# Optimization experiments

Measured on AMD Instinct MI355X. Metric: run time of the kernel, lower is better.

Reference implementation:

```python
import jax, jax.numpy as jnp
import numpy as np

NEG_INF = -9e15
ALPHA = 0.2  # leaky relu slope


def setup_inputs() -> dict:
    key = jax.random.key(0)
    k1, k2, k3, k4 = jax.random.split(key, 4)
    B, N, Din = 8, 1024, 128
    H, D = 8, 16
    h = jax.random.normal(k1, (B, N, Din), dtype=jnp.float32)
    adj = jax.random.randint(k2, (B, N, N), 0, 2, dtype=jnp.int32)
    W = jax.random.normal(k3, (Din, H * D), dtype=jnp.float32) * 0.1
    a = jax.random.normal(k4, (H, 2 * D, 1), dtype=jnp.float32) * 0.1
    return {"h": h, "adj": adj, "W": W, "a": a}


def reference(h, adj, W, a):
    B, N, _ = h.shape
    H, twoD, _ = a.shape
    D = twoD // 2
    # Wh: [B, N, H, D]
    Wh = (h @ W).reshape(B, N, H, D)
    # Decompose additive attention: a . [Wh_i ; Wh_j] = a_src . Wh_i + a_dst . Wh_j
    a_src = a[:, :D, 0]   # [H, D]
    a_dst = a[:, D:, 0]   # [H, D]
    s_i = jnp.einsum('bnhd,hd->bhn', Wh, a_src)  # [B, H, N]
    s_j = jnp.einsum('bnhd,hd->bhn', Wh, a_dst)  # [B, H, N]
    scores = jax.nn.leaky_relu(s_i[:, :, :, None] + s_j[:, :, None, :], ALPHA)  # [B,H,N,N]
    scores = jnp.where(adj[:, None, :, :] == 0, NEG_INF, scores)
    attn = jax.nn.softmax(scores, axis=-1)  # [B, H, N, N]
    # Weighted aggregation over neighbors j
    h_prime = jnp.einsum('bhij,bjhd->bihd', attn, Wh).reshape(B, N, H * D)
    return h_prime
```

## Files before the change

kernel.cpp:

```cpp
#include <hip/hip_runtime.h>
#include <hip/hip_bf16.h>

constexpr int B   = 8;
constexpr int N   = 1024;
constexpr int DIN = 128;
constexpr int H   = 8;
constexpr int D   = 16;
constexpr int HD  = 128;
constexpr int TI  = 16;

#define LOG2E 1.4426950408889634f
#define TCLAMP 30.0f

typedef __attribute__((ext_vector_type(8))) short bf16x8;
typedef __attribute__((ext_vector_type(4))) float f32x4;

__device__ inline float fast_exp2(float x) {
#if __has_builtin(__builtin_amdgcn_exp2f)
    return __builtin_amdgcn_exp2f(x);
#else
    return exp2f(x);
#endif
}

__global__ __launch_bounds__(256) void k_proj(
    const float* __restrict__ hsrc,
    const float* __restrict__ W,
    const float* __restrict__ a,
    __hip_bfloat16* __restrict__ WhT,
    float* __restrict__ tI,
    float* __restrict__ tJ)
{
    const int row0 = blockIdx.x * 16;
    const int b    = row0 >> 10;
    const int n0   = row0 & (N - 1);
    const int t    = threadIdx.x;
    const int lane = t & 63, wave = t >> 6;
    const int mn   = lane & 15, kg = lane >> 4;

    __shared__ __align__(16) __hip_bfloat16 hA[16][136];
    __shared__ __align__(16) __hip_bfloat16 Wt[128][136];

    {
        const float4* hf = reinterpret_cast<const float4*>(hsrc + (size_t)row0 * DIN);
        #pragma unroll
        for (int u = 0; u < 2; ++u) {
            const int idx = t + u * 256;
            const float4 v = hf[idx];
            const int r = idx >> 5, c4 = (idx & 31) * 4;
            hA[r][c4]     = __float2bfloat16(v.x);
            hA[r][c4 + 1] = __float2bfloat16(v.y);
            hA[r][c4 + 2] = __float2bfloat16(v.z);
            hA[r][c4 + 3] = __float2bfloat16(v.w);
        }
    }
    {
        const float4* wf = reinterpret_cast<const float4*>(W);
        #pragma unroll
        for (int u = 0; u < 16; ++u) {
            const int idx = t + u * 256;
            const float4 v = wf[idx];
            const int k = idx >> 5, c0 = (idx & 31) * 4;
            Wt[c0][k]     = __float2bfloat16(v.x);
            Wt[c0 + 1][k] = __float2bfloat16(v.y);
            Wt[c0 + 2][k] = __float2bfloat16(v.z);
            Wt[c0 + 3][k] = __float2bfloat16(v.w);
        }
    }
    __syncthreads();

    f32x4 acc[2];
    acc[0] = (f32x4){0.f, 0.f, 0.f, 0.f};
    acc[1] = (f32x4){0.f, 0.f, 0.f, 0.f};

    #pragma unroll
    for (int kk = 0; kk < 4; ++kk) {
        const bf16x8 af = *reinterpret_cast<const bf16x8*>(
            &hA[mn][kk * 32 + kg * 8]);
        #pragma unroll
        for (int f = 0; f < 2; ++f) {
            const int F = wave * 2 + f;
            const bf16x8 bfr = *reinterpret_cast<const bf16x8*>(
                &Wt[F * 16 + mn][kk * 32 + kg * 8]);
            acc[f] = __builtin_amdgcn_mfma_f32_16x16x32_bf16(af, bfr, acc[f], 0, 0, 0);
        }
    }

    #pragma unroll
    for (int f = 0; f < 2; ++f) {
        const int F = wave * 2 + f;
        const float as = a[F * 32 + mn];
        const float ad = a[F * 32 + 16 + mn];
        #pragma unroll
        for (int r = 0; r < 4; ++r) {
            const int n = n0 + kg * 4 + r;
            WhT[((size_t)(b * HD + F * 16 + mn)) * N + n] =
                __float2bfloat16(acc[f][r]);
            float vi = acc[f][r] * as;
            float vj = acc[f][r] * ad;
            #pragma unroll
            for (int m = 1; m < 16; m <<= 1) {
                vi += __shfl_xor(vi, m);
                vj += __shfl_xor(vj, m);
            }
            if (mn == 0) {
                tI[((size_t)(b * H + F)) * N + n] = fminf(vi * LOG2E, TCLAMP);
                tJ[((size_t)(b * H + F)) * N + n] = fminf(vj * LOG2E, TCLAMP);
            }
        }
    }
}

__global__ __launch_bounds__(512, 4) void k_attn(
    const int*            __restrict__ adj,
    const __hip_bfloat16* __restrict__ WhT,
    const float*          __restrict__ tI,
    const float*          __restrict__ tJ,
    float*                __restrict__ out)
{
    const int b    = blockIdx.y;
    const int i0   = blockIdx.x * TI;
    const int t    = threadIdx.x;
    const int lane = t & 63, h = t >> 6;
    const int mn   = lane & 15, kg = lane >> 4;

    __shared__ unsigned int m2[32][16];

    {
        const int* ar = adj + ((size_t)(b * N) + i0 + 2 * h) * N + lane;
        #pragma unroll
        for (int rr = 0; rr < 2; ++rr) {
            #pragma unroll
            for (int tt = 0; tt < 16; ++tt) {
                const int v = ar[rr * N + tt * 64];
                const unsigned long long mm = __ballot(v != 0);
                if (lane == 0)
                    m2[2 * tt][2 * h + rr] = (unsigned int)mm;
                if (lane == 32)
                    m2[2 * tt + 1][2 * h + rr] = (unsigned int)(mm >> 32);
            }
        }
    }
    __syncthreads();

    const float Arow = tI[((size_t)(b * H + h)) * N + i0 + mn];
    const float* tjrow = tJ + ((size_t)(b * H + h)) * N + kg * 8;
    const __hip_bfloat16* wrow =
        WhT + ((size_t)(b * HD + h * 16 + mn)) * N + kg * 8;

    f32x4 accO = {0.f, 0.f, 0.f, 0.f};
    f32x4 accD = {0.f, 0.f, 0.f, 0.f};
    bf16x8 ones;
    #pragma unroll
    for (int e = 0; e < 8; ++e) ones[e] = (short)0x3F80;

    for (int sq = 0; sq < 8; ++sq) {
        const int j0 = sq * 128;

        unsigned int mvq[4];
        #pragma unroll
        for (int q = 0; q < 4; ++q) mvq[q] = m2[sq * 4 + q][mn];
        float4 ta[4], tb[4]; bf16x8 wv[4];
        #pragma unroll
        for (int q = 0; q < 4; ++q) {
            ta[q] = *reinterpret_cast<const float4*>(tjrow + j0 + q * 32);
            tb[q] = *reinterpret_cast<const float4*>(tjrow + j0 + q * 32 + 4);
            wv[q] = *reinterpret_cast<const bf16x8*>(wrow + j0 + q * 32);
        }

        #pragma unroll
        for (int q = 0; q < 4; ++q) {
            const unsigned int m8 = (mvq[q] >> (kg * 8)) & 0xFFu;
            const float tv[8] = {ta[q].x, ta[q].y, ta[q].z, ta[q].w,
                                 tb[q].x, tb[q].y, tb[q].z, tb[q].w};
            bf16x8 af;
            #pragma unroll
            for (int e = 0; e < 8; ++e) {
                const float x = Arow + tv[e];
                float sc = fmaxf(x, 0.2f * x);
                sc = ((m8 >> e) & 1u) ? sc : -1.0e30f;
                af[e] = (short)__bfloat16_as_ushort(
                    __float2bfloat16(fast_exp2(sc)));
            }
            accO = __builtin_amdgcn_mfma_f32_16x16x32_bf16(af, wv[q], accO, 0, 0, 0);
            accD = __builtin_amdgcn_mfma_f32_16x16x32_bf16(af, ones, accD, 0, 0, 0);
        }
    }

    #pragma unroll
    for (int r = 0; r < 4; ++r) {
        out[((size_t)(b * N) + i0 + kg * 4 + r) * HD + h * 16 + mn] =
            accO[r] / accD[r];
    }
}

extern "C" void kernel_launch(void* const* d_in, const int* in_sizes, int n_in,
                              void* d_out, int out_size, void* d_ws, size_t ws_size,
                              hipStream_t stream)
{
    const float* h   = (const float*)d_in[0];
    const int*   adj = (const int*)d_in[1];
    const float* W   = (const float*)d_in[2];
    const float* a   = (const float*)d_in[3];
    float* out = (float*)d_out;

    float* ws = (float*)d_ws;
    float* tI = ws;
    float* tJ = ws + (size_t)B * H * N;
    __hip_bfloat16* WhT = (__hip_bfloat16*)(ws + (size_t)2 * B * H * N);

    k_proj<<<dim3(B * N / 16), dim3(256), 0, stream>>>(h, W, a, WhT, tI, tJ);
    k_attn<<<dim3(N / TI, B), dim3(512), 0, stream>>>(adj, WhT, tI, tJ, out);
}
```

Baseline: 55.10 us.

## Pre-pack adjacency bitmask in separate kernel and double-buffer loads in attention

Adjacency ballot-packing moves out of the attention kernel into a dedicated k_pack kernel that writes a per-row 32-word bitmask. The attention kernel now reads this bitmask straight from global memory, with no shared memory or block barrier. Its grid is split over head halves to give 256-thread blocks. The j-loop is double-buffered with two register sets, and sched_barriers overlap the next chunk's loads with the current chunk's compute. This costs an extra kernel launch and more register pressure, and it drops the previous occupancy hint.

```diff
diff --git a/kernel.cpp b/kernel.cpp
--- a/kernel.cpp
+++ b/kernel.cpp
@@ -21,6 +21,21 @@
 #else
     return exp2f(x);
 #endif
+}
+
+__global__ __launch_bounds__(256) void k_pack(const int* __restrict__ adj,
+                                              unsigned int* __restrict__ bm)
+{
+    const int lane = threadIdx.x & 63;
+    const size_t row = (size_t)blockIdx.x * 4 + (threadIdx.x >> 6);
+    const int* ar = adj + row * N + lane;
+    unsigned int* dst = bm + row * 32;
+    #pragma unroll
+    for (int tt = 0; tt < 16; ++tt) {
+        const unsigned long long m = __ballot(ar[tt * 64] != 0);
+        if (lane == 0)  dst[2 * tt]     = (unsigned int)m;
+        if (lane == 32) dst[2 * tt + 1] = (unsigned int)(m >> 32);
+    }
 }
 
 __global__ __launch_bounds__(256) void k_proj(
@@ -111,8 +126,38 @@
     }
 }
 
-__global__ __launch_bounds__(512, 4) void k_attn(
-    const int*            __restrict__ adj,
+
+#define LOADSET(M, T0, T1, WV, SQ) do {                                        \
+    M = mrow[SQ];                                                              \
+    _Pragma("unroll")                                                          \
+    for (int q = 0; q < 4; ++q) {                                              \
+        T0[q] = *reinterpret_cast<const float4*>(tjrow + (SQ) * 128 + q * 32);     \
+        T1[q] = *reinterpret_cast<const float4*>(tjrow + (SQ) * 128 + q * 32 + 4); \
+        WV[q] = *reinterpret_cast<const bf16x8*>(wrow + (SQ) * 128 + q * 32);      \
+    } } while (0)
+
+#define COMPUTESET(M, T0, T1, WV) do {                                         \
+    const unsigned int mq_[4] = {M.x, M.y, M.z, M.w};                          \
+    _Pragma("unroll")                                                          \
+    for (int q = 0; q < 4; ++q) {                                              \
+        const unsigned int m8_ = (mq_[q] >> (kg * 8)) & 0xFFu;                 \
+        const float tv_[8] = {T0[q].x, T0[q].y, T0[q].z, T0[q].w,              \
+                              T1[q].x, T1[q].y, T1[q].z, T1[q].w};             \
+        bf16x8 af_;                                                            \
+        _Pragma("unroll")                                                      \
+        for (int e = 0; e < 8; ++e) {                                          \
+            const float x_ = Arow + tv_[e];                                    \
+            float sc_ = fmaxf(x_, 0.2f * x_);                                  \
+            sc_ = ((m8_ >> e) & 1u) ? sc_ : -1.0e30f;                          \
+            af_[e] = (short)__bfloat16_as_ushort(                              \
+                __float2bfloat16(fast_exp2(sc_)));                             \
+        }                                                                      \
+        accO = __builtin_amdgcn_mfma_f32_16x16x32_bf16(af_, WV[q], accO, 0, 0, 0); \
+        accD = __builtin_amdgcn_mfma_f32_16x16x32_bf16(af_, ones, accD, 0, 0, 0);  \
+    } } while (0)
+
+__global__ __launch_bounds__(256) void k_attn(
+    const unsigned int*   __restrict__ bm,
     const __hip_bfloat16* __restrict__ WhT,
     const float*          __restrict__ tI,
     const float*          __restrict__ tJ,
@@ -120,33 +165,17 @@
 {
     const int b    = blockIdx.y;
     const int i0   = blockIdx.x * TI;
-    const int t    = threadIdx.x;
-    const int lane = t & 63, h = t >> 6;
+    const int lane = threadIdx.x & 63;
+    const int h    = blockIdx.z * 4 + (threadIdx.x >> 6);
     const int mn   = lane & 15, kg = lane >> 4;
-
-    __shared__ unsigned int m2[32][16];
-
-    {
-        const int* ar = adj + ((size_t)(b * N) + i0 + 2 * h) * N + lane;
-        #pragma unroll
-        for (int rr = 0; rr < 2; ++rr) {
-            #pragma unroll
-            for (int tt = 0; tt < 16; ++tt) {
-                const int v = ar[rr * N + tt * 64];
-                const unsigned long long mm = __ballot(v != 0);
-                if (lane == 0)
-                    m2[2 * tt][2 * h + rr] = (unsigned int)mm;
-                if (lane == 32)
-                    m2[2 * tt + 1][2 * h + rr] = (unsigned int)(mm >> 32);
-            }
-        }
-    }
-    __syncthreads();
-
-    const float Arow = tI[((size_t)(b * H + h)) * N + i0 + mn];
+    const int row  = i0 + mn;
+
+    const float Arow = tI[((size_t)(b * H + h)) * N + row];
     const float* tjrow = tJ + ((size_t)(b * H + h)) * N + kg * 8;
     const __hip_bfloat16* wrow =
         WhT + ((size_t)(b * HD + h * 16 + mn)) * N + kg * 8;
+    const uint4* mrow = reinterpret_cast<const uint4*>(
+        bm + ((size_t)(b * N) + row) * 32);
 
     f32x4 accO = {0.f, 0.f, 0.f, 0.f};
     f32x4 accD = {0.f, 0.f, 0.f, 0.f};
@@ -154,37 +183,20 @@
     #pragma unroll
     for (int e = 0; e < 8; ++e) ones[e] = (short)0x3F80;
 
-    for (int sq = 0; sq < 8; ++sq) {
-        const int j0 = sq * 128;
-
-        unsigned int mvq[4];
-        #pragma unroll
-        for (int q = 0; q < 4; ++q) mvq[q] = m2[sq * 4 + q][mn];
-        float4 ta[4], tb[4]; bf16x8 wv[4];
-        #pragma unroll
-        for (int q = 0; q < 4; ++q) {
-            ta[q] = *reinterpret_cast<const float4*>(tjrow + j0 + q * 32);
-            tb[q] = *reinterpret_cast<const float4*>(tjrow + j0 + q * 32 + 4);
-            wv[q] = *reinterpret_cast<const bf16x8*>(wrow + j0 + q * 32);
-        }
-
-        #pragma unroll
-        for (int q = 0; q < 4; ++q) {
-            const unsigned int m8 = (mvq[q] >> (kg * 8)) & 0xFFu;
-            const float tv[8] = {ta[q].x, ta[q].y, ta[q].z, ta[q].w,
-                                 tb[q].x, tb[q].y, tb[q].z, tb[q].w};
-            bf16x8 af;
-            #pragma unroll
-            for (int e = 0; e < 8; ++e) {
-                const float x = Arow + tv[e];
-                float sc = fmaxf(x, 0.2f * x);
-                sc = ((m8 >> e) & 1u) ? sc : -1.0e30f;
-                af[e] = (short)__bfloat16_as_ushort(
-                    __float2bfloat16(fast_exp2(sc)));
-            }
-            accO = __builtin_amdgcn_mfma_f32_16x16x32_bf16(af, wv[q], accO, 0, 0, 0);
-            accD = __builtin_amdgcn_mfma_f32_16x16x32_bf16(af, ones, accD, 0, 0, 0);
-        }
+    uint4 mA; float4 taA[4], tbA[4]; bf16x8 wvA[4];
+    uint4 mB; float4 taB[4], tbB[4]; bf16x8 wvB[4];
+
+    LOADSET(mA, taA, tbA, wvA, 0);
+    #pragma unroll
+    for (int s2 = 0; s2 < 4; ++s2) {
+        LOADSET(mB, taB, tbB, wvB, 2 * s2 + 1);
+        __builtin_amdgcn_sched_barrier(0);
+        COMPUTESET(mA, taA, tbA, wvA);
+        if (s2 < 3) {
+            LOADSET(mA, taA, tbA, wvA, 2 * s2 + 2);
+        }
+        __builtin_amdgcn_sched_barrier(0);
+        COMPUTESET(mB, taB, tbB, wvB);
     }
 
     #pragma unroll
@@ -208,7 +220,10 @@
     float* tI = ws;
     float* tJ = ws + (size_t)B * H * N;
     __hip_bfloat16* WhT = (__hip_bfloat16*)(ws + (size_t)2 * B * H * N);
-
+    unsigned int* bm = (unsigned int*)((char*)WhT +
+                       (size_t)B * N * HD * sizeof(__hip_bfloat16));
+
+    k_pack<<<dim3(B * N / 4), dim3(256), 0, stream>>>(adj, bm);
     k_proj<<<dim3(B * N / 16), dim3(256), 0, stream>>>(h, W, a, WhT, tI, tJ);
-    k_attn<<<dim3(N / TI, B), dim3(512), 0, stream>>>(adj, WhT, tI, tJ, out);
-}
+    k_attn<<<dim3(N / TI, B, 2), dim3(256), 0, stream>>>(bm, WhT, tI, tJ, out);
+}
```

Measured after the change: 52.82 us. 4.1% less time.

## Prepack adjacency bitmask in separate kernel and split attention across heads and j-halves

Applied to the files above, without the earlier changes.

A new pre-pass kernel packs the int32 adjacency matrix into a bitmask in workspace, so the attention kernel no longer does per-block ballots and LDS staging. The attention kernel now launches one block per (row tile, batch, head) with two waves that each cover half of the neighbor dimension, then combines the partial numerators and denominators through shared memory. This raises the block count and shortens the per-wave serial loop. In exchange it adds an extra kernel launch plus a write and read of the bitmask, and each head's block re-reads the same mask rows.

```diff
diff --git a/kernel.cpp b/kernel.cpp
--- a/kernel.cpp
+++ b/kernel.cpp
@@ -21,6 +21,21 @@
 #else
     return exp2f(x);
 #endif
+}
+
+__global__ __launch_bounds__(256) void k_pack(const int* __restrict__ adj,
+                                              unsigned int* __restrict__ bm)
+{
+    const int lane = threadIdx.x & 63;
+    const size_t row = (size_t)blockIdx.x * 4 + (threadIdx.x >> 6);
+    const int* ar = adj + row * N + lane;
+    unsigned int* dst = bm + row * 32;
+    #pragma unroll
+    for (int tt = 0; tt < 16; ++tt) {
+        const unsigned long long m = __ballot(ar[tt * 64] != 0);
+        if (lane == 0)  dst[2 * tt]     = (unsigned int)m;
+        if (lane == 32) dst[2 * tt + 1] = (unsigned int)(m >> 32);
+    }
 }
 
 __global__ __launch_bounds__(256) void k_proj(
@@ -111,8 +126,8 @@
     }
 }
 
-__global__ __launch_bounds__(512, 4) void k_attn(
-    const int*            __restrict__ adj,
+__global__ __launch_bounds__(128, 8) void k_attn(
+    const unsigned int*   __restrict__ bm,
     const __hip_bfloat16* __restrict__ WhT,
     const float*          __restrict__ tI,
     const float*          __restrict__ tJ,
@@ -120,33 +135,18 @@
 {
     const int b    = blockIdx.y;
     const int i0   = blockIdx.x * TI;
-    const int t    = threadIdx.x;
-    const int lane = t & 63, h = t >> 6;
+    const int h    = blockIdx.z;
+    const int wv   = threadIdx.x >> 6;
+    const int lane = threadIdx.x & 63;
     const int mn   = lane & 15, kg = lane >> 4;
-
-    __shared__ unsigned int m2[32][16];
-
-    {
-        const int* ar = adj + ((size_t)(b * N) + i0 + 2 * h) * N + lane;
-        #pragma unroll
-        for (int rr = 0; rr < 2; ++rr) {
-            #pragma unroll
-            for (int tt = 0; tt < 16; ++tt) {
-                const int v = ar[rr * N + tt * 64];
-                const unsigned long long mm = __ballot(v != 0);
-                if (lane == 0)
-                    m2[2 * tt][2 * h + rr] = (unsigned int)mm;
-                if (lane == 32)
-                    m2[2 * tt + 1][2 * h + rr] = (unsigned int)(mm >> 32);
-            }
-        }
-    }
-    __syncthreads();
-
-    const float Arow = tI[((size_t)(b * H + h)) * N + i0 + mn];
-    const float* tjrow = tJ + ((size_t)(b * H + h)) * N + kg * 8;
+    const int row  = i0 + mn;
+
+    const float Arow = tI[((size_t)(b * H + h)) * N + row];
+    const float* tjrow = tJ + ((size_t)(b * H + h)) * N + wv * 512 + kg * 8;
     const __hip_bfloat16* wrow =
-        WhT + ((size_t)(b * HD + h * 16 + mn)) * N + kg * 8;
+        WhT + ((size_t)(b * HD + h * 16 + mn)) * N + wv * 512 + kg * 8;
+    const unsigned int* mrow =
+        bm + ((size_t)(b * N) + row) * 32 + wv * 16;
 
     f32x4 accO = {0.f, 0.f, 0.f, 0.f};
     f32x4 accD = {0.f, 0.f, 0.f, 0.f};
@@ -154,43 +154,44 @@
     #pragma unroll
     for (int e = 0; e < 8; ++e) ones[e] = (short)0x3F80;
 
-    for (int sq = 0; sq < 8; ++sq) {
-        const int j0 = sq * 128;
-
-        unsigned int mvq[4];
-        #pragma unroll
-        for (int q = 0; q < 4; ++q) mvq[q] = m2[sq * 4 + q][mn];
-        float4 ta[4], tb[4]; bf16x8 wv[4];
-        #pragma unroll
-        for (int q = 0; q < 4; ++q) {
-            ta[q] = *reinterpret_cast<const float4*>(tjrow + j0 + q * 32);
-            tb[q] = *reinterpret_cast<const float4*>(tjrow + j0 + q * 32 + 4);
-            wv[q] = *reinterpret_cast<const bf16x8*>(wrow + j0 + q * 32);
-        }
-
-        #pragma unroll
-        for (int q = 0; q < 4; ++q) {
-            const unsigned int m8 = (mvq[q] >> (kg * 8)) & 0xFFu;
-            const float tv[8] = {ta[q].x, ta[q].y, ta[q].z, ta[q].w,
-                                 tb[q].x, tb[q].y, tb[q].z, tb[q].w};
-            bf16x8 af;
-            #pragma unroll
-            for (int e = 0; e < 8; ++e) {
-                const float x = Arow + tv[e];
-                float sc = fmaxf(x, 0.2f * x);
-                sc = ((m8 >> e) & 1u) ? sc : -1.0e30f;
-                af[e] = (short)__bfloat16_as_ushort(
-                    __float2bfloat16(fast_exp2(sc)));
-            }
-            accO = __builtin_amdgcn_mfma_f32_16x16x32_bf16(af, wv[q], accO, 0, 0, 0);
-            accD = __builtin_amdgcn_mfma_f32_16x16x32_bf16(af, ones, accD, 0, 0, 0);
-        }
-    }
-
-    #pragma unroll
-    for (int r = 0; r < 4; ++r) {
-        out[((size_t)(b * N) + i0 + kg * 4 + r) * HD + h * 16 + mn] =
-            accO[r] / accD[r];
+    #pragma unroll 4
+    for (int s = 0; s < 16; ++s) {
+        const unsigned int m8 = (mrow[s] >> (kg * 8)) & 0xFFu;
+        const float4 t0 = *reinterpret_cast<const float4*>(tjrow + s * 32);
+        const float4 t1 = *reinterpret_cast<const float4*>(tjrow + s * 32 + 4);
+        const bf16x8 wfr = *reinterpret_cast<const bf16x8*>(wrow + s * 32);
+
+        const float tv[8] = {t0.x, t0.y, t0.z, t0.w, t1.x, t1.y, t1.z, t1.w};
+        bf16x8 af;
+        #pragma unroll
+        for (int e = 0; e < 8; ++e) {
+            const float x = Arow + tv[e];
+            float sc = fmaxf(x, 0.2f * x);
+            sc = ((m8 >> e) & 1u) ? sc : -1.0e30f;
+            af[e] = (short)__bfloat16_as_ushort(
+                __float2bfloat16(fast_exp2(sc)));
+        }
+        accO = __builtin_amdgcn_mfma_f32_16x16x32_bf16(af, wfr, accO, 0, 0, 0);
+        accD = __builtin_amdgcn_mfma_f32_16x16x32_bf16(af, ones, accD, 0, 0, 0);
+    }
+
+    __shared__ float redO[64][4];
+    __shared__ float redD[64][4];
+    if (wv == 1) {
+        #pragma unroll
+        for (int r = 0; r < 4; ++r) {
+            redO[lane][r] = accO[r];
+            redD[lane][r] = accD[r];
+        }
+    }
+    __syncthreads();
+    if (wv == 0) {
+        #pragma unroll
+        for (int r = 0; r < 4; ++r) {
+            const float o = accO[r] + redO[lane][r];
+            const float d = accD[r] + redD[lane][r];
+            out[((size_t)(b * N) + i0 + kg * 4 + r) * HD + h * 16 + mn] = o / d;
+        }
     }
 }
 
@@ -208,7 +209,10 @@
     float* tI = ws;
     float* tJ = ws + (size_t)B * H * N;
     __hip_bfloat16* WhT = (__hip_bfloat16*)(ws + (size_t)2 * B * H * N);
-
+    unsigned int* bm = (unsigned int*)((char*)WhT +
+                       (size_t)B * N * HD * sizeof(__hip_bfloat16));
+
+    k_pack<<<dim3(B * N / 4), dim3(256), 0, stream>>>(adj, bm);
     k_proj<<<dim3(B * N / 16), dim3(256), 0, stream>>>(h, W, a, WhT, tI, tJ);
-    k_attn<<<dim3(N / TI, B), dim3(512), 0, stream>>>(adj, WhT, tI, tJ, out);
-}
+    k_attn<<<dim3(N / TI, B, H), dim3(128), 0, stream>>>(bm, WhT, tI, tJ, out);
+}
```

Result: faster. 53.06 us (-3.7%).
